# Performance work log

Measured on AMD Instinct MI355X. Metric: run time of the kernel, lower is better.

Reference implementation:

```python
import jax, jax.numpy as jnp
import numpy as np

B, D, U = 64, 256, 256

def setup_inputs() -> dict:
    key = jax.random.key(0)
    ks = jax.random.split(key, 16)
    init_mu = 0.05
    inputs = jax.random.normal(ks[0], (B, D), jnp.float32)
    prev_state = 0.1 * jax.random.normal(ks[1], (B, U), jnp.float32)
    A = jax.random.normal(ks[2], (B, U, U), jnp.float32)
    # symmetric, diagonally boosted covariance-like state
    Sigma_state = 0.01 * (A + jnp.swapaxes(A, 1, 2)) + 0.1 * jnp.eye(U, dtype=jnp.float32)
    def w(k, shape):
        return init_mu * jax.random.normal(k, shape, jnp.float32)
    def s(k):
        return jax.random.uniform(k, (U,), jnp.float32, -4.5, -2.2)
    return {
        'inputs': inputs, 'prev_state': prev_state, 'Sigma_state': Sigma_state,
        'U_z': w(ks[3], (D, U)), 'uz_sigma': s(ks[4]), 'W_z': w(ks[5], (U, U)), 'wz_sigma': s(ks[6]),
        'U_r': w(ks[7], (D, U)), 'ur_sigma': s(ks[8]), 'W_r': w(ks[9], (U, U)), 'wr_sigma': s(ks[10]),
        'U_h': w(ks[11], (D, U)), 'uh_sigma': s(ks[12]), 'W_h': w(ks[13], (U, U)), 'wh_sigma': s(ks[14]),
    }

def _outer(a, b):  # [B,u],[B,u] -> [B,u,u]
    return a[:, :, None] * b[:, None, :]

def _quad(W, S):  # W^T @ S @ W, S is [B,u,u]
    return jnp.matmul(jnp.matmul(W.T, S), W)

def _x_sigma_w(x, sv):  # ||x||^2 * diag(softplus sigma)
    return jnp.sum(x * x, axis=1)[:, None, None] * jnp.diag(sv)

def _tr_sigma_w(S, sv):  # trace(S) * diag(softplus sigma)
    return jnp.trace(S, axis1=1, axis2=2)[:, None, None] * jnp.diag(sv)

def _hadamard_sigma(S1, S2, m1, m2):
    # S1*S2 + diag(m1) S2 diag(m1) + diag(m2) S1 diag(m2) as elementwise/broadcast
    return S1 * S2 + _outer(m1, m1) * S2 + _outer(m2, m2) * S1

def reference(inputs, prev_state, Sigma_state, U_z, uz_sigma, W_z, wz_sigma,
              U_r, ur_sigma, W_r, wr_sigma, U_h, uh_sigma, W_h, wh_sigma):
    sp = jax.nn.softplus
    # --- z gate ---
    az = inputs @ U_z + prev_state @ W_z
    z = jax.nn.sigmoid(az)
    gz = z * (1.0 - z)  # d sigmoid
    Sz = (_quad(W_z, Sigma_state) + _x_sigma_w(prev_state, sp(wz_sigma))
          + _tr_sigma_w(Sigma_state, sp(wz_sigma)) + _x_sigma_w(inputs, sp(uz_sigma)))
    Sigma_out_z = Sz * _outer(gz, gz)
    # --- r gate ---
    ar = inputs @ U_r + prev_state @ W_r
    r = jax.nn.sigmoid(ar)
    gr = r * (1.0 - r)
    Sr = (_quad(W_r, Sigma_state) + _x_sigma_w(prev_state, sp(wr_sigma))
          + _tr_sigma_w(Sigma_state, sp(wr_sigma)) + _x_sigma_w(inputs, sp(ur_sigma)))
    Sigma_out_r = Sr * _outer(gr, gr)
    # --- h candidate ---
    g_in = prev_state * r
    ah = inputs @ U_h + g_in @ W_h
    h = jnp.tanh(ah)
    gh = 1.0 - h * h  # d tanh
    sigma_g = _hadamard_sigma(Sigma_state, Sigma_out_r, prev_state, r)
    Sh = (_quad(W_h, sigma_g) + _x_sigma_w(g_in, sp(wh_sigma))
          + _tr_sigma_w(sigma_g, sp(wh_sigma)) + _x_sigma_w(inputs, sp(uh_sigma)))
    Sigma_out_h = Sh * _outer(gh, gh)
    # --- output combination ---
    mu_out = z * prev_state + (1.0 - z) * h
    sigma_a = _hadamard_sigma(Sigma_out_z, Sigma_state, z, prev_state)
    sigma_b = _hadamard_sigma(Sigma_out_z, Sigma_out_h, 1.0 - z, h)
    Sigma_out = (sigma_a + sigma_b
                 - Sigma_out_z * _outer(prev_state, h)
                 - Sigma_out_z * _outer(h, prev_state))
    Sigma_out = jnp.where(jnp.isnan(Sigma_out) | jnp.isinf(Sigma_out),
                          jnp.zeros_like(Sigma_out), Sigma_out)
    eye = jnp.eye(Sigma_out.shape[-1], dtype=Sigma_out.dtype)
    d = jnp.abs(jnp.diagonal(Sigma_out, axis1=1, axis2=2))
    Sigma_out = Sigma_out * (1.0 - eye) + d[:, :, None] * eye
    return mu_out, Sigma_out
```

## Files before the change

kernel.cpp:

```cpp
#include <hip/hip_runtime.h>
#include <math.h>

#define UDIM 256
#define BATCH 64
#define MATN 65536
#define PITCH 280

typedef __bf16 bf16x8 __attribute__((ext_vector_type(8)));
typedef float  f32x4  __attribute__((ext_vector_type(4)));

__device__ __forceinline__ float softplusf(float x) { return log1pf(expf(x)); }
__device__ __forceinline__ float sigmoidf_(float x) { return 1.f/(1.f+expf(-x)); }

__device__ __forceinline__ bf16x8 frag_load(const __bf16* base, int rt, int kt, int lane) {
  return *(const bf16x8*)(base + (((size_t)(rt*8 + kt))*64 + lane)*8);
}

__device__ __forceinline__ bf16x8 cvt8(const float* p) {
  const float4 f0 = *(const float4*)p;
  const float4 f1 = *(const float4*)(p + 4);
  bf16x8 v;
  v[0]=(__bf16)f0.x; v[1]=(__bf16)f0.y; v[2]=(__bf16)f0.z; v[3]=(__bf16)f0.w;
  v[4]=(__bf16)f1.x; v[5]=(__bf16)f1.y; v[6]=(__bf16)f1.z; v[7]=(__bf16)f1.w;
  return v;
}

__global__ __launch_bounds__(256) void prep_all(
    const float* __restrict__ Uz, const float* __restrict__ Wz,
    const float* __restrict__ Ur, const float* __restrict__ Wr,
    const float* __restrict__ Uh, const float* __restrict__ Wh,
    __bf16* __restrict__ Fw_z, __bf16* __restrict__ Fw_r,
    __bf16* __restrict__ Fu_h, __bf16* __restrict__ Fw_h,
    const float* __restrict__ S, const float* __restrict__ x,
    const float* __restrict__ prev, float* __restrict__ scal,
    __bf16* __restrict__ Sf,
    float* __restrict__ zb, float* __restrict__ rb,
    float* __restrict__ gzb, float* __restrict__ grb,
    float* __restrict__ gin)
{
  const int bid = blockIdx.x;
  const int t = threadIdx.x;
  const int w = t >> 6, l = t & 63, r = l & 15, q = l >> 4;

  __shared__ __align__(16) unsigned char LDSU[16896];

  if (bid < 1024) {
    const int c = bid;
    const int bx = c & 3, by = (c >> 2) & 3, b = c >> 4;
    const size_t sb = (size_t)b * MATN;
#pragma unroll
    for (int ss = 0; ss < 2; ++ss) {
      const int s = t + ss*256;
      const int chunk = s >> 6, lane = s & 63;
      const int rt_l = chunk >> 1, kt_l = chunk & 1;
      const int row = by*64 + rt_l*16 + (lane & 15);
      const int col = bx*64 + kt_l*32 + (lane >> 4)*8;
      const bf16x8 v = cvt8(S + sb + (size_t)row*UDIM + col);
      *(bf16x8*)(Sf + sb + (((size_t)((by*4 + rt_l)*8 + bx*2 + kt_l))*64 + lane)*8) = v;
    }
    return;
  }

  if (bid < 1088) {
    const int u3 = bid - 1024;
    const int mat = u3 >> 4, tl = u3 & 15;
    const int n0 = (tl & 3)*64, k0 = (tl >> 2)*64;
    const float* W; __bf16* F;
    switch (mat) {
      case 0: W = Wz; F = Fw_z; break;  case 1: W = Wr; F = Fw_r; break;
      case 2: W = Uh; F = Fu_h; break;  default: W = Wh; F = Fw_h; break;
    }
    float (*tile)[65] = (float (*)[65])LDSU;
    const int tx = t & 15, ty = t >> 4;
#pragma unroll
    for (int rr = 0; rr < 4; ++rr) {
      const int row = ty*4 + rr;
      const float4 f = *(const float4*)(W + (size_t)(k0 + row)*UDIM + n0 + tx*4);
      tile[row][tx*4+0] = f.x; tile[row][tx*4+1] = f.y;
      tile[row][tx*4+2] = f.z; tile[row][tx*4+3] = f.w;
    }
    __syncthreads();
#pragma unroll
    for (int ss = 0; ss < 2; ++ss) {
      const int s = t + ss*256;
      const int rt_l = s >> 7, kt_l = (s >> 6) & 1, lane = s & 63;
      const int nl = rt_l*16 + (lane & 15), kb = kt_l*32 + (lane >> 4)*8;
      __align__(16) __bf16 tmp[8];
#pragma unroll
      for (int e = 0; e < 8; ++e) tmp[e] = (__bf16)tile[kb + e][nl];
      *(uint4*)(F + (((size_t)((((n0 >> 4) + rt_l)*8) + (k0 >> 5) + kt_l))*64 + lane)*8)
          = *(const uint4*)tmp;
    }
    return;
  }

  if (bid < 1104) {
    const int blk = bid - 1088;
    const int b0 = blk*4 + (t >> 6);
    const float4 xv = *(const float4*)(x + b0*UDIM + l*4);
    float s0 = xv.x*xv.x + xv.y*xv.y + xv.z*xv.z + xv.w*xv.w;
    const float4 pv = *(const float4*)(prev + b0*UDIM + l*4);
    float s1 = pv.x*pv.x + pv.y*pv.y + pv.z*pv.z + pv.w*pv.w;
    float s2 = 0.f;
#pragma unroll
    for (int e = 0; e < 4; ++e)
      s2 += S[(size_t)b0*MATN + (size_t)(l*4 + e)*257];
    for (int off = 32; off; off >>= 1) {
      s0 += __shfl_down(s0, off);
      s1 += __shfl_down(s1, off);
      s2 += __shfl_down(s2, off);
    }
    if (l == 0) { scal[b0] = s0; scal[64 + b0] = s1; scal[128 + b0] = s2; }
    return;
  }

  {
    const int u2 = bid - 1104;
    const int g = u2 >> 4, un = u2 & 15;
    const int jt = un >> 2, ni = un & 3;
    const int n0 = un * 16;
    const float* Um = g ? Ur : Uz;
    const float* Wm = g ? Wr : Wz;
    __bf16 (*Ut)[16][264] = (__bf16 (*)[16][264])LDSU;
    {
      float uv[16], wv[16];
      const float* ur_ = Um + (size_t)t*UDIM + n0;
      const float* wr_ = Wm + (size_t)t*UDIM + n0;
#pragma unroll
      for (int p4 = 0; p4 < 4; ++p4) {
        *(float4*)&uv[p4*4] = *(const float4*)(ur_ + p4*4);
        *(float4*)&wv[p4*4] = *(const float4*)(wr_ + p4*4);
      }
#pragma unroll
      for (int e = 0; e < 16; ++e) {
        Ut[0][e][t] = (__bf16)uv[e];
        Ut[1][e][t] = (__bf16)wv[e];
      }
    }
    __syncthreads();

    const int mrow = w*16 + r;
    f32x4 acc = {};
#pragma unroll
    for (int ks = 0; ks < 16; ++ks) {
      const int k0 = ks*32;
      const float* asrc;
      int src, koff;
      if (k0 < 256) { asrc = x    + (size_t)mrow*UDIM + k0         + q*8; src = 0; koff = k0; }
      else          { asrc = prev + (size_t)mrow*UDIM + (k0 - 256) + q*8; src = 1; koff = k0 - 256; }
      const bf16x8 af = cvt8(asrc);
      const bf16x8 bv = *(const bf16x8*)&Ut[src][r][koff + q*8];
      acc = __builtin_amdgcn_mfma_f32_16x16x32_bf16(af, bv, acc, 0, 0, 0);
    }
    const int n = n0 + r;
    if (g == 0) {
#pragma unroll
      for (int v = 0; v < 4; ++v) {
        const int m = w*16 + q*4 + v;
        const float zv = sigmoidf_(acc[v]);
        zb[m*UDIM + n]  = zv;
        gzb[m*UDIM + n] = zv * (1.f - zv);
      }
    } else {
      float ggp[4];
#pragma unroll
      for (int v = 0; v < 4; ++v) {
        const int m = w*16 + q*4 + v;
        const float rv = sigmoidf_(acc[v]);
        const float pv = prev[m*UDIM + n];
        const float g2 = pv * rv;
        rb[m*UDIM + n]  = rv;
        grb[m*UDIM + n] = rv * (1.f - rv);
        gin[m*UDIM + n] = g2;
        ggp[v] = g2 * g2;
      }
#pragma unroll
      for (int s2 = 1; s2 < 16; s2 <<= 1)
#pragma unroll
        for (int v = 0; v < 4; ++v) ggp[v] += __shfl_xor(ggp[v], s2);
      if (r == 0)
#pragma unroll
        for (int v = 0; v < 4; ++v)
          atomicAdd(&scal[192 + w*16 + q*4 + v], ggp[v]);
    }
  }
}

__global__ __launch_bounds__(256, 4) void quad_zr_gh(
    const float* __restrict__ S, const __bf16* __restrict__ Sf,
    const float* __restrict__ prev,
    const float* __restrict__ rb, const float* __restrict__ gzb,
    const float* __restrict__ grb,
    const float* __restrict__ wz_s, const float* __restrict__ uz_s,
    const float* __restrict__ wr_s, const float* __restrict__ ur_s,
    const __bf16* __restrict__ Fw_z, const __bf16* __restrict__ Fw_r,
    float* __restrict__ scal, __bf16* __restrict__ Szb, __bf16* __restrict__ G,
    const float* __restrict__ x, const float* __restrict__ gin,
    const float* __restrict__ zb,
    const __bf16* __restrict__ Fu_h, const __bf16* __restrict__ Fw_h,
    float* __restrict__ hb, float* __restrict__ ghb, float* __restrict__ mu_out)
{
  const int bid = blockIdx.x;
  const int t = threadIdx.x, w = t >> 6, l = t & 63, r = l & 15, q = l >> 4;

  if (bid < 4) {
    const int jt = bid;
    const int mrow = w*16 + r;
    f32x4 acc[4] = {};
#pragma unroll
    for (int ks = 0; ks < 16; ++ks) {
      const int k0 = ks*32;
      const float* asrc; const __bf16* B; int kk;
      if (k0 < 256) { asrc = x   + (size_t)mrow*UDIM + k0         + q*8; B = Fu_h; kk = k0; }
      else          { asrc = gin + (size_t)mrow*UDIM + (k0 - 256) + q*8; B = Fw_h; kk = k0 - 256; }
      const bf16x8 af = cvt8(asrc);
#pragma unroll
      for (int ni = 0; ni < 4; ++ni) {
        const bf16x8 bv = frag_load(B, jt*4 + ni, kk >> 5, l);
        acc[ni] = __builtin_amdgcn_mfma_f32_16x16x32_bf16(af, bv, acc[ni], 0, 0, 0);
      }
    }
#pragma unroll
    for (int ni = 0; ni < 4; ++ni) {
      const int n = jt*64 + ni*16 + r;
#pragma unroll
      for (int v = 0; v < 4; ++v) {
        const int m = w*16 + q*4 + v;
        const float hv = tanhf(acc[ni][v]);
        const float zv = zb[m*UDIM + n];
        hb[m*UDIM + n]  = hv;
        ghb[m*UDIM + n] = 1.f - hv*hv;
        mu_out[m*UDIM + n] = zv * prev[m*UDIM + n] + (1.f - zv) * hv;
      }
    }
    return;
  }

  const int id = bid - 4;
  const int gater = (id < 1024);
  const int rem = id & 1023;
  const int s = rem >> 6, b = rem & 63;
  const size_t sb = (size_t)b * MATN;
  const __bf16* Sfb = Sf + sb;
  const __bf16* FW = gater ? Fw_r : Fw_z;

  __shared__ __align__(16) __bf16 T[16*PITCH];

  f32x4 a[4] = {};
#pragma unroll
  for (int kt = 0; kt < 8; ++kt) {
    const bf16x8 af = frag_load(FW, s, kt, l);
#pragma unroll
    for (int ct = 0; ct < 4; ++ct) {
      const bf16x8 bv = frag_load(Sfb, w*4 + ct, kt, l);
      a[ct] = __builtin_amdgcn_mfma_f32_16x16x32_bf16(af, bv, a[ct], 0, 0, 0);
    }
  }
#pragma unroll
  for (int ct = 0; ct < 4; ++ct)
#pragma unroll
    for (int v = 0; v < 4; ++v)
      T[(q*4 + v)*PITCH + w*64 + ct*16 + r] = (__bf16)a[ct][v];
  __syncthreads();

  f32x4 qx[4] = {};
#pragma unroll
  for (int kt = 0; kt < 8; ++kt) {
    const bf16x8 at = *(const bf16x8*)&T[r*PITCH + kt*32 + q*8];
#pragma unroll
    for (int ct = 0; ct < 4; ++ct) {
      const bf16x8 bw = frag_load(FW, w*4 + ct, kt, l);
      qx[ct] = __builtin_amdgcn_mfma_f32_16x16x32_bf16(at, bw, qx[ct], 0, 0, 0);
    }
  }

  const float xx = scal[b];
  const float dscal = scal[64 + b] + scal[128 + b];
  const int ib = s*16 + q*4;

  if (!gater) {
    const f32x4 g4 = *(const f32x4*)(gzb + b*UDIM + ib);
    __align__(16) __bf16 o16[16];
#pragma unroll
    for (int ct = 0; ct < 4; ++ct) {
      const int j = (w*4 + ct)*16 + r;
      const float gj = gzb[b*UDIM + j];
#pragma unroll
      for (int v = 0; v < 4; ++v) {
        const int i = ib + v;
        float qv = qx[ct][v];
        if (i == j) qv += dscal*softplusf(wz_s[i]) + xx*softplusf(uz_s[i]);
        o16[ct*4 + v] = (__bf16)(qv * g4[v] * gj);
      }
    }
    __bf16* dst = Szb + ((size_t)(b*16 + s)*256 + t)*16;
    *(uint4*)dst       = *(const uint4*)&o16[0];
    *(uint4*)(dst + 8) = *(const uint4*)&o16[8];
  } else {
    float gvals[16];
    float trg = 0.f;
    {
      const f32x4 g4 = *(const f32x4*)(grb + b*UDIM + ib);
      const f32x4 p4 = *(const f32x4*)(prev + b*UDIM + ib);
      const f32x4 r4 = *(const f32x4*)(rb + b*UDIM + ib);
#pragma unroll
      for (int ct = 0; ct < 4; ++ct) {
        const int j = (w*4 + ct)*16 + r;
        const float gj = grb[b*UDIM + j];
        const float pj = prev[b*UDIM + j];
        const float rj = rb[b*UDIM + j];
#pragma unroll
        for (int v = 0; v < 4; ++v) {
          const int i = ib + v;
          float qv = qx[ct][v];
          if (i == j) qv += dscal*softplusf(wr_s[i]) + xx*softplusf(ur_s[i]);
          const float Sg = qv * g4[v] * gj;
          const float sv = S[sb + (size_t)i*UDIM + j];
          const float go = Sg*(sv + p4[v]*pj) + r4[v]*rj*sv;
          gvals[ct*4 + v] = go;
          if (i == j) trg += go;
        }
      }
    }
    if (trg != 0.f) atomicAdd(&scal[256 + b], trg);

    __syncthreads();
#pragma unroll
    for (int ct = 0; ct < 4; ++ct)
#pragma unroll
      for (int v = 0; v < 4; ++v)
        T[(q*4 + v)*PITCH + w*64 + ct*16 + r] = (__bf16)gvals[ct*4 + v];
    __syncthreads();
#pragma unroll
    for (int ee = 0; ee < 2; ++ee) {
      const int e = t + ee*256;
      const int kt = e >> 6, le = e & 63;
      const uint4 vv = *(const uint4*)&T[(le & 15)*PITCH + kt*32 + (le >> 4)*8];
      *(uint4*)(G + sb + (((size_t)(s*8 + kt))*64 + le)*8) = vv;
    }
  }
}

__global__ __launch_bounds__(256, 4) void quad_h(
    const float* __restrict__ S, const __bf16* __restrict__ Szb,
    const float* __restrict__ prev, const float* __restrict__ zb,
    const float* __restrict__ hb, const float* __restrict__ ghb,
    const float* __restrict__ wh_s, const float* __restrict__ uh_s,
    const __bf16* __restrict__ Fw_h, const __bf16* __restrict__ G,
    const float* __restrict__ scal, float* __restrict__ out_sig)
{
  const int bid = blockIdx.x;
  const int s = bid >> 6, b = bid & 63;
  const size_t sb = (size_t)b * MATN;
  const int t = threadIdx.x, w = t >> 6, l = t & 63, r = l & 15, q = l >> 4;
  const __bf16* Gb = G + sb;

  __shared__ __align__(16) __bf16 Th[16*PITCH];

  f32x4 ah[4] = {};
#pragma unroll
  for (int kt = 0; kt < 8; ++kt) {
    const bf16x8 af = frag_load(Fw_h, s, kt, l);
#pragma unroll
    for (int ct = 0; ct < 4; ++ct) {
      const bf16x8 bv = frag_load(Gb, w*4 + ct, kt, l);
      ah[ct] = __builtin_amdgcn_mfma_f32_16x16x32_bf16(af, bv, ah[ct], 0, 0, 0);
    }
  }
#pragma unroll
  for (int ct = 0; ct < 4; ++ct)
#pragma unroll
    for (int v = 0; v < 4; ++v)
      Th[(q*4 + v)*PITCH + w*64 + ct*16 + r] = (__bf16)ah[ct][v];
  __syncthreads();

  f32x4 qh[4] = {};
#pragma unroll
  for (int kt = 0; kt < 8; ++kt) {
    const bf16x8 at = *(const bf16x8*)&Th[r*PITCH + kt*32 + q*8];
#pragma unroll
    for (int ct = 0; ct < 4; ++ct) {
      const bf16x8 bv = frag_load(Fw_h, w*4 + ct, kt, l);
      qh[ct] = __builtin_amdgcn_mfma_f32_16x16x32_bf16(at, bv, qh[ct], 0, 0, 0);
    }
  }

  const float xx = scal[b];
  const float dscal = scal[192 + b] + scal[256 + b];
  const int ib = s*16 + q*4;

  const __bf16* szp = Szb + ((size_t)(b*16 + s)*256 + t)*16;
  __align__(16) __bf16 sz16[16];
  *(uint4*)&sz16[0] = *(const uint4*)szp;
  *(uint4*)&sz16[8] = *(const uint4*)(szp + 8);

  const f32x4 g4 = *(const f32x4*)(ghb + b*UDIM + ib);
  const f32x4 p4 = *(const f32x4*)(prev + b*UDIM + ib);
  const f32x4 z4 = *(const f32x4*)(zb + b*UDIM + ib);
  const f32x4 h4 = *(const f32x4*)(hb + b*UDIM + ib);

#pragma unroll
  for (int ct = 0; ct < 4; ++ct) {
    const int j = (w*4 + ct)*16 + r;
    const float gj = ghb[b*UDIM + j];
    const float pj = prev[b*UDIM + j];
    const float zj = zb[b*UDIM + j];
    const float hj = hb[b*UDIM + j];
#pragma unroll
    for (int v = 0; v < 4; ++v) {
      const int i = ib + v;
      float qv = qh[ct][v];
      if (i == j) qv += dscal*softplusf(wh_s[i]) + xx*softplusf(uh_s[i]);
      const float Sg = qv * g4[v] * gj;
      const float sv = S[sb + (size_t)i*UDIM + j];
      const float sz = (float)sz16[ct*4 + v];
      float val = sv*(sz + z4[v]*zj)
                + sz*(p4[v] - h4[v])*(pj - hj)
                + Sg*(sz + (1.f - z4[v])*(1.f - zj));
      if (!isfinite(val)) val = 0.f;
      if (i == j) val = fabsf(val);
      out_sig[sb + (size_t)i*UDIM + j] = val;
    }
  }
}

extern "C" void kernel_launch(void* const* d_in, const int* in_sizes, int n_in,
                              void* d_out, int out_size, void* d_ws, size_t ws_size,
                              hipStream_t stream) {
  const float* x    = (const float*)d_in[0];
  const float* prev = (const float*)d_in[1];
  const float* S    = (const float*)d_in[2];
  const float* Uz   = (const float*)d_in[3];
  const float* uz_s = (const float*)d_in[4];
  const float* Wz   = (const float*)d_in[5];
  const float* wz_s = (const float*)d_in[6];
  const float* Ur   = (const float*)d_in[7];
  const float* ur_s = (const float*)d_in[8];
  const float* Wr   = (const float*)d_in[9];
  const float* wr_s = (const float*)d_in[10];
  const float* Uh   = (const float*)d_in[11];
  const float* uh_s = (const float*)d_in[12];
  const float* Wh   = (const float*)d_in[13];
  const float* wh_s = (const float*)d_in[14];

  float* out_mu  = (float*)d_out;
  float* out_sig = out_mu + BATCH*UDIM;

  float* ws   = (float*)d_ws;
  float* zb   = ws;
  float* rb   = zb  + BATCH*UDIM;
  float* gzb  = rb  + BATCH*UDIM;
  float* grb  = gzb + BATCH*UDIM;
  float* gin  = grb + BATCH*UDIM;
  float* hb   = gin + BATCH*UDIM;
  float* ghb  = hb  + BATCH*UDIM;
  float* scal = ghb + BATCH*UDIM;
  __bf16* bws  = (__bf16*)(scal + 512);
  __bf16* Fu_z = bws;
  __bf16* Fw_z = Fu_z + MATN;
  __bf16* Fu_r = Fw_z + MATN;
  __bf16* Fw_r = Fu_r + MATN;
  __bf16* Fu_h = Fw_r + MATN;
  __bf16* Fw_h = Fu_h + MATN;
  const size_t BIG = (size_t)BATCH * MATN;
  __bf16* Szb = Fw_h + MATN;
  __bf16* G   = Szb + BIG;
  __bf16* Sf  = G + BIG;

  (void)hipMemsetAsync(scal, 0, 512*sizeof(float), stream);

  prep_all<<<dim3(1136), 256, 0, stream>>>(Uz, Wz, Ur, Wr, Uh, Wh,
      Fw_z, Fw_r, Fu_h, Fw_h, S, x, prev, scal, Sf,
      zb, rb, gzb, grb, gin);
  quad_zr_gh<<<dim3(2052), 256, 0, stream>>>(S, Sf, prev, rb, gzb, grb,
      wz_s, uz_s, wr_s, ur_s, Fw_z, Fw_r, scal, Szb, G,
      x, gin, zb, Fu_h, Fw_h, hb, ghb, out_mu);
  quad_h<<<dim3(1024), 256, 0, stream>>>(S, Szb, prev, zb, hb, ghb,
      wh_s, uh_s, Fw_h, G, scal, out_sig);
}
```

Measured before the change: 166.0 us.

## Drop bf16 Sigma pre-pack and process two row slabs per block

```diff
diff --git a/kernel.cpp b/kernel.cpp
--- a/kernel.cpp
+++ b/kernel.cpp
@@ -23,6 +23,12 @@
   v[0]=(__bf16)f0.x; v[1]=(__bf16)f0.y; v[2]=(__bf16)f0.z; v[3]=(__bf16)f0.w;
   v[4]=(__bf16)f1.x; v[5]=(__bf16)f1.y; v[6]=(__bf16)f1.z; v[7]=(__bf16)f1.w;
   return v;
+}
+
+__device__ __forceinline__ bf16x8 sfrag(const float* Sb, int rt, int kt, int lane) {
+  const int row = rt*16 + (lane & 15);
+  const int col = kt*32 + (lane >> 4)*8;
+  return cvt8(Sb + (size_t)row*UDIM + col);
 }
 
 __global__ __launch_bounds__(256) void prep_all(
@@ -33,7 +39,6 @@
     __bf16* __restrict__ Fu_h, __bf16* __restrict__ Fw_h,
     const float* __restrict__ S, const float* __restrict__ x,
     const float* __restrict__ prev, float* __restrict__ scal,
-    __bf16* __restrict__ Sf,
     float* __restrict__ zb, float* __restrict__ rb,
     float* __restrict__ gzb, float* __restrict__ grb,
     float* __restrict__ gin)
@@ -44,26 +49,8 @@
 
   __shared__ __align__(16) unsigned char LDSU[16896];
 
-  if (bid < 1024) {
-    const int c = bid;
-    const int bx = c & 3, by = (c >> 2) & 3, b = c >> 4;
-    const size_t sb = (size_t)b * MATN;
-#pragma unroll
-    for (int ss = 0; ss < 2; ++ss) {
-      const int s = t + ss*256;
-      const int chunk = s >> 6, lane = s & 63;
-      const int rt_l = chunk >> 1, kt_l = chunk & 1;
-      const int row = by*64 + rt_l*16 + (lane & 15);
-      const int col = bx*64 + kt_l*32 + (lane >> 4)*8;
-      const bf16x8 v = cvt8(S + sb + (size_t)row*UDIM + col);
-      *(bf16x8*)(Sf + sb + (((size_t)((by*4 + rt_l)*8 + bx*2 + kt_l))*64 + lane)*8) = v;
-    }
-    return;
-  }
-
-  if (bid < 1088) {
-    const int u3 = bid - 1024;
-    const int mat = u3 >> 4, tl = u3 & 15;
+  if (bid < 64) {
+    const int mat = bid >> 4, tl = bid & 15;
     const int n0 = (tl & 3)*64, k0 = (tl >> 2)*64;
     const float* W; __bf16* F;
     switch (mat) {
@@ -94,8 +81,8 @@
     return;
   }
 
-  if (bid < 1104) {
-    const int blk = bid - 1088;
+  if (bid < 80) {
+    const int blk = bid - 64;
     const int b0 = blk*4 + (t >> 6);
     const float4 xv = *(const float4*)(x + b0*UDIM + l*4);
     float s0 = xv.x*xv.x + xv.y*xv.y + xv.z*xv.z + xv.w*xv.w;
@@ -115,9 +102,8 @@
   }
 
   {
-    const int u2 = bid - 1104;
+    const int u2 = bid - 80;
     const int g = u2 >> 4, un = u2 & 15;
-    const int jt = un >> 2, ni = un & 3;
     const int n0 = un * 16;
     const float* Um = g ? Ur : Uz;
     const float* Wm = g ? Wr : Wz;
@@ -187,7 +173,7 @@
 }
 
 __global__ __launch_bounds__(256, 4) void quad_zr_gh(
-    const float* __restrict__ S, const __bf16* __restrict__ Sf,
+    const float* __restrict__ S,
     const float* __restrict__ prev,
     const float* __restrict__ rb, const float* __restrict__ gzb,
     const float* __restrict__ grb,
@@ -237,69 +223,86 @@
   }
 
   const int id = bid - 4;
-  const int gater = (id < 1024);
-  const int rem = id & 1023;
-  const int s = rem >> 6, b = rem & 63;
+  const int gater = (id < 512);
+  const int rem = id & 511;
+  const int sg = rem >> 6, b = rem & 63;
   const size_t sb = (size_t)b * MATN;
-  const __bf16* Sfb = Sf + sb;
+  const float* Sb = S + sb;
   const __bf16* FW = gater ? Fw_r : Fw_z;
 
-  __shared__ __align__(16) __bf16 T[16*PITCH];
-
-  f32x4 a[4] = {};
+  __shared__ __align__(16) __bf16 T[2*16*PITCH];
+
+  f32x4 a[2][4] = {};
 #pragma unroll
   for (int kt = 0; kt < 8; ++kt) {
-    const bf16x8 af = frag_load(FW, s, kt, l);
+    bf16x8 af2[2];
+#pragma unroll
+    for (int sl = 0; sl < 2; ++sl) af2[sl] = frag_load(FW, sg*2 + sl, kt, l);
 #pragma unroll
     for (int ct = 0; ct < 4; ++ct) {
-      const bf16x8 bv = frag_load(Sfb, w*4 + ct, kt, l);
-      a[ct] = __builtin_amdgcn_mfma_f32_16x16x32_bf16(af, bv, a[ct], 0, 0, 0);
-    }
-  }
-#pragma unroll
-  for (int ct = 0; ct < 4; ++ct)
-#pragma unroll
-    for (int v = 0; v < 4; ++v)
-      T[(q*4 + v)*PITCH + w*64 + ct*16 + r] = (__bf16)a[ct][v];
+      const bf16x8 bv = sfrag(Sb, w*4 + ct, kt, l);
+#pragma unroll
+      for (int sl = 0; sl < 2; ++sl)
+        a[sl][ct] = __builtin_amdgcn_mfma_f32_16x16x32_bf16(af2[sl], bv, a[sl][ct], 0, 0, 0);
+    }
+  }
+#pragma unroll
+  for (int sl = 0; sl < 2; ++sl)
+#pragma unroll
+    for (int ct = 0; ct < 4; ++ct)
+#pragma unroll
+      for (int v = 0; v < 4; ++v)
+        T[sl*16*PITCH + (q*4 + v)*PITCH + w*64 + ct*16 + r] = (__bf16)a[sl][ct][v];
   __syncthreads();
 
-  f32x4 qx[4] = {};
+  f32x4 qx[2][4] = {};
 #pragma unroll
   for (int kt = 0; kt < 8; ++kt) {
-    const bf16x8 at = *(const bf16x8*)&T[r*PITCH + kt*32 + q*8];
-#pragma unroll
-    for (int ct = 0; ct < 4; ++ct) {
-      const bf16x8 bw = frag_load(FW, w*4 + ct, kt, l);
-      qx[ct] = __builtin_amdgcn_mfma_f32_16x16x32_bf16(at, bw, qx[ct], 0, 0, 0);
+    bf16x8 bw[4];
+#pragma unroll
+    for (int ct = 0; ct < 4; ++ct) bw[ct] = frag_load(FW, w*4 + ct, kt, l);
+#pragma unroll
+    for (int sl = 0; sl < 2; ++sl) {
+      const bf16x8 at = *(const bf16x8*)&T[sl*16*PITCH + r*PITCH + kt*32 + q*8];
+#pragma unroll
+      for (int ct = 0; ct < 4; ++ct)
+        qx[sl][ct] = __builtin_amdgcn_mfma_f32_16x16x32_bf16(at, bw[ct], qx[sl][ct], 0, 0, 0);
     }
   }
 
   const float xx = scal[b];
   const float dscal = scal[64 + b] + scal[128 + b];
-  const int ib = s*16 + q*4;
 
   if (!gater) {
-    const f32x4 g4 = *(const f32x4*)(gzb + b*UDIM + ib);
-    __align__(16) __bf16 o16[16];
-#pragma unroll
-    for (int ct = 0; ct < 4; ++ct) {
-      const int j = (w*4 + ct)*16 + r;
-      const float gj = gzb[b*UDIM + j];
-#pragma unroll
-      for (int v = 0; v < 4; ++v) {
-        const int i = ib + v;
-        float qv = qx[ct][v];
-        if (i == j) qv += dscal*softplusf(wz_s[i]) + xx*softplusf(uz_s[i]);
-        o16[ct*4 + v] = (__bf16)(qv * g4[v] * gj);
-      }
-    }
-    __bf16* dst = Szb + ((size_t)(b*16 + s)*256 + t)*16;
-    *(uint4*)dst       = *(const uint4*)&o16[0];
-    *(uint4*)(dst + 8) = *(const uint4*)&o16[8];
+#pragma unroll
+    for (int sl = 0; sl < 2; ++sl) {
+      const int s4 = sg*2 + sl;
+      const int ib = s4*16 + q*4;
+      const f32x4 g4 = *(const f32x4*)(gzb + b*UDIM + ib);
+      __align__(16) __bf16 o16[16];
+#pragma unroll
+      for (int ct = 0; ct < 4; ++ct) {
+        const int j = (w*4 + ct)*16 + r;
+        const float gj = gzb[b*UDIM + j];
+#pragma unroll
+        for (int v = 0; v < 4; ++v) {
+          const int i = ib + v;
+          float qv = qx[sl][ct][v];
+          if (i == j) qv += dscal*softplusf(wz_s[i]) + xx*softplusf(uz_s[i]);
+          o16[ct*4 + v] = (__bf16)(qv * g4[v] * gj);
+        }
+      }
+      __bf16* dst = Szb + ((size_t)(b*16 + s4)*256 + t)*16;
+      *(uint4*)dst       = *(const uint4*)&o16[0];
+      *(uint4*)(dst + 8) = *(const uint4*)&o16[8];
+    }
   } else {
-    float gvals[16];
+    __syncthreads();
     float trg = 0.f;
-    {
+#pragma unroll
+    for (int sl = 0; sl < 2; ++sl) {
+      const int s4 = sg*2 + sl;
+      const int ib = s4*16 + q*4;
       const f32x4 g4 = *(const f32x4*)(grb + b*UDIM + ib);
       const f32x4 p4 = *(const f32x4*)(prev + b*UDIM + ib);
       const f32x4 r4 = *(const f32x4*)(rb + b*UDIM + ib);
@@ -312,32 +315,27 @@
 #pragma unroll
         for (int v = 0; v < 4; ++v) {
           const int i = ib + v;
-          float qv = qx[ct][v];
+          float qv = qx[sl][ct][v];
           if (i == j) qv += dscal*softplusf(wr_s[i]) + xx*softplusf(ur_s[i]);
           const float Sg = qv * g4[v] * gj;
-          const float sv = S[sb + (size_t)i*UDIM + j];
+          const float sv = Sb[(size_t)i*UDIM + j];
           const float go = Sg*(sv + p4[v]*pj) + r4[v]*rj*sv;
-          gvals[ct*4 + v] = go;
+          T[sl*16*PITCH + (q*4 + v)*PITCH + w*64 + ct*16 + r] = (__bf16)go;
           if (i == j) trg += go;
         }
       }
     }
     if (trg != 0.f) atomicAdd(&scal[256 + b], trg);
-
     __syncthreads();
 #pragma unroll
-    for (int ct = 0; ct < 4; ++ct)
-#pragma unroll
-      for (int v = 0; v < 4; ++v)
-        T[(q*4 + v)*PITCH + w*64 + ct*16 + r] = (__bf16)gvals[ct*4 + v];
-    __syncthreads();
-#pragma unroll
-    for (int ee = 0; ee < 2; ++ee) {
-      const int e = t + ee*256;
-      const int kt = e >> 6, le = e & 63;
-      const uint4 vv = *(const uint4*)&T[(le & 15)*PITCH + kt*32 + (le >> 4)*8];
-      *(uint4*)(G + sb + (((size_t)(s*8 + kt))*64 + le)*8) = vv;
-    }
+    for (int sl = 0; sl < 2; ++sl)
+#pragma unroll
+      for (int ee = 0; ee < 2; ++ee) {
+        const int e = t + ee*256;
+        const int kt = e >> 6, le = e & 63;
+        const uint4 vv = *(const uint4*)&T[sl*16*PITCH + (le & 15)*PITCH + kt*32 + (le >> 4)*8];
+        *(uint4*)(G + sb + (((size_t)((sg*2 + sl)*8 + kt))*64 + le)*8) = vv;
+      }
   }
 }
 
@@ -350,76 +348,91 @@
     const float* __restrict__ scal, float* __restrict__ out_sig)
 {
   const int bid = blockIdx.x;
-  const int s = bid >> 6, b = bid & 63;
+  const int sg = bid >> 6, b = bid & 63;
   const size_t sb = (size_t)b * MATN;
   const int t = threadIdx.x, w = t >> 6, l = t & 63, r = l & 15, q = l >> 4;
   const __bf16* Gb = G + sb;
 
-  __shared__ __align__(16) __bf16 Th[16*PITCH];
-
-  f32x4 ah[4] = {};
+  __shared__ __align__(16) __bf16 Th[2*16*PITCH];
+
+  f32x4 ah[2][4] = {};
 #pragma unroll
   for (int kt = 0; kt < 8; ++kt) {
-    const bf16x8 af = frag_load(Fw_h, s, kt, l);
+    bf16x8 af2[2];
+#pragma unroll
+    for (int sl = 0; sl < 2; ++sl) af2[sl] = frag_load(Fw_h, sg*2 + sl, kt, l);
 #pragma unroll
     for (int ct = 0; ct < 4; ++ct) {
       const bf16x8 bv = frag_load(Gb, w*4 + ct, kt, l);
-      ah[ct] = __builtin_amdgcn_mfma_f32_16x16x32_bf16(af, bv, ah[ct], 0, 0, 0);
-    }
-  }
-#pragma unroll
-  for (int ct = 0; ct < 4; ++ct)
-#pragma unroll
-    for (int v = 0; v < 4; ++v)
-      Th[(q*4 + v)*PITCH + w*64 + ct*16 + r] = (__bf16)ah[ct][v];
+#pragma unroll
+      for (int sl = 0; sl < 2; ++sl)
+        ah[sl][ct] = __builtin_amdgcn_mfma_f32_16x16x32_bf16(af2[sl], bv, ah[sl][ct], 0, 0, 0);
+    }
+  }
+#pragma unroll
+  for (int sl = 0; sl < 2; ++sl)
+#pragma unroll
+    for (int ct = 0; ct < 4; ++ct)
+#pragma unroll
+      for (int v = 0; v < 4; ++v)
+        Th[sl*16*PITCH + (q*4 + v)*PITCH + w*64 + ct*16 + r] = (__bf16)ah[sl][ct][v];
   __syncthreads();
 
-  f32x4 qh[4] = {};
+  f32x4 qh[2][4] = {};
 #pragma unroll
   for (int kt = 0; kt < 8; ++kt) {
-    const bf16x8 at = *(const bf16x8*)&Th[r*PITCH + kt*32 + q*8];
-#pragma unroll
-    for (int ct = 0; ct < 4; ++ct) {
-      const bf16x8 bv = frag_load(Fw_h, w*4 + ct, kt, l);
-      qh[ct] = __builtin_amdgcn_mfma_f32_16x16x32_bf16(at, bv, qh[ct], 0, 0, 0);
+    bf16x8 bw2[4];
+#pragma unroll
+    for (int ct = 0; ct < 4; ++ct) bw2[ct] = frag_load(Fw_h, w*4 + ct, kt, l);
+#pragma unroll
+    for (int sl = 0; sl < 2; ++sl) {
+      const bf16x8 at = *(const bf16x8*)&Th[sl*16*PITCH + r*PITCH + kt*32 + q*8];
+#pragma unroll
+      for (int ct = 0; ct < 4; ++ct)
+        qh[sl][ct] = __builtin_amdgcn_mfma_f32_16x16x32_bf16(at, bw2[ct], qh[sl][ct], 0, 0, 0);
     }
   }
 
   const float xx = scal[b];
   const float dscal = scal[192 + b] + scal[256 + b];
-  const int ib = s*16 + q*4;
-
-  const __bf16* szp = Szb + ((size_t)(b*16 + s)*256 + t)*16;
-  __align__(16) __bf16 sz16[16];
-  *(uint4*)&sz16[0] = *(const uint4*)szp;
-  *(uint4*)&sz16[8] = *(const uint4*)(szp + 8);
-
-  const f32x4 g4 = *(const f32x4*)(ghb + b*UDIM + ib);
-  const f32x4 p4 = *(const f32x4*)(prev + b*UDIM + ib);
-  const f32x4 z4 = *(const f32x4*)(zb + b*UDIM + ib);
-  const f32x4 h4 = *(const f32x4*)(hb + b*UDIM + ib);
-
-#pragma unroll
-  for (int ct = 0; ct < 4; ++ct) {
-    const int j = (w*4 + ct)*16 + r;
-    const float gj = ghb[b*UDIM + j];
-    const float pj = prev[b*UDIM + j];
-    const float zj = zb[b*UDIM + j];
-    const float hj = hb[b*UDIM + j];
-#pragma unroll
-    for (int v = 0; v < 4; ++v) {
-      const int i = ib + v;
-      float qv = qh[ct][v];
-      if (i == j) qv += dscal*softplusf(wh_s[i]) + xx*softplusf(uh_s[i]);
-      const float Sg = qv * g4[v] * gj;
-      const float sv = S[sb + (size_t)i*UDIM + j];
-      const float sz = (float)sz16[ct*4 + v];
-      float val = sv*(sz + z4[v]*zj)
-                + sz*(p4[v] - h4[v])*(pj - hj)
-                + Sg*(sz + (1.f - z4[v])*(1.f - zj));
-      if (!isfinite(val)) val = 0.f;
-      if (i == j) val = fabsf(val);
-      out_sig[sb + (size_t)i*UDIM + j] = val;
+
+#pragma unroll
+  for (int sl = 0; sl < 2; ++sl) {
+    const int s4 = sg*2 + sl;
+    const int ib = s4*16 + q*4;
+
+    const __bf16* szp = Szb + ((size_t)(b*16 + s4)*256 + t)*16;
+    __align__(16) __bf16 sz16[16];
+    *(uint4*)&sz16[0] = *(const uint4*)szp;
+    *(uint4*)&sz16[8] = *(const uint4*)(szp + 8);
+
+    const f32x4 g4 = *(const f32x4*)(ghb + b*UDIM + ib);
+    const f32x4 p4 = *(const f32x4*)(prev + b*UDIM + ib);
+    const f32x4 z4 = *(const f32x4*)(zb + b*UDIM + ib);
+    const f32x4 h4 = *(const f32x4*)(hb + b*UDIM + ib);
+
+#pragma unroll
+    for (int ct = 0; ct < 4; ++ct) {
+      const int j = (w*4 + ct)*16 + r;
+      const float gj = ghb[b*UDIM + j];
+      const float pj = prev[b*UDIM + j];
+      const float zj = zb[b*UDIM + j];
+      const float hj = hb[b*UDIM + j];
+#pragma unroll
+      for (int v = 0; v < 4; ++v) {
+        const int i = ib + v;
+        float qv = qh[sl][ct][v];
+        if (i == j) qv += dscal*softplusf(wh_s[i]) + xx*softplusf(uh_s[i]);
+        const float Sg = qv * g4[v] * gj;
+        const float sv = S[sb + (size_t)i*UDIM + j];
+        const float sz = (float)sz16[ct*4 + v];
+        float val = sv*(sz + z4[v]*zj)
+                  + sz*(p4[v] - h4[v])*(pj - hj)
+                  + Sg*(sz + (1.f - z4[v])*(1.f - zj));
+        if (!isfinite(val)) val = 0.f;
+        if (i == j) val = fabsf(val);
+        out_sig[sb + (size_t)i*UDIM + j] = val;
+      }
     }
   }
 }
@@ -456,25 +469,22 @@
   float* ghb  = hb  + BATCH*UDIM;
   float* scal = ghb + BATCH*UDIM;
   __bf16* bws  = (__bf16*)(scal + 512);
-  __bf16* Fu_z = bws;
-  __bf16* Fw_z = Fu_z + MATN;
-  __bf16* Fu_r = Fw_z + MATN;
-  __bf16* Fw_r = Fu_r + MATN;
+  __bf16* Fw_z = bws;
+  __bf16* Fw_r = Fw_z + MATN;
   __bf16* Fu_h = Fw_r + MATN;
   __bf16* Fw_h = Fu_h + MATN;
   const size_t BIG = (size_t)BATCH * MATN;
   __bf16* Szb = Fw_h + MATN;
   __bf16* G   = Szb + BIG;
-  __bf16* Sf  = G + BIG;
 
   (void)hipMemsetAsync(scal, 0, 512*sizeof(float), stream);
 
-  prep_all<<<dim3(1136), 256, 0, stream>>>(Uz, Wz, Ur, Wr, Uh, Wh,
-      Fw_z, Fw_r, Fu_h, Fw_h, S, x, prev, scal, Sf,
+  prep_all<<<dim3(112), 256, 0, stream>>>(Uz, Wz, Ur, Wr, Uh, Wh,
+      Fw_z, Fw_r, Fu_h, Fw_h, S, x, prev, scal,
       zb, rb, gzb, grb, gin);
-  quad_zr_gh<<<dim3(2052), 256, 0, stream>>>(S, Sf, prev, rb, gzb, grb,
+  quad_zr_gh<<<dim3(1028), 256, 0, stream>>>(S, prev, rb, gzb, grb,
       wz_s, uz_s, wr_s, ur_s, Fw_z, Fw_r, scal, Szb, G,
       x, gin, zb, Fu_h, Fw_h, hb, ghb, out_mu);
-  quad_h<<<dim3(1024), 256, 0, stream>>>(S, Szb, prev, zb, hb, ghb,
+  quad_h<<<dim3(512), 256, 0, stream>>>(S, Szb, prev, zb, hb, ghb,
       wh_s, uh_s, Fw_h, G, scal, out_sig);
 }
```

Result: slower. 178.9 us (+7.7%).

## Compute z and r gate quadratic forms in one block sharing Sigma fragments

Applied to the files above, without the earlier changes.

```diff
diff --git a/kernel.cpp b/kernel.cpp
--- a/kernel.cpp
+++ b/kernel.cpp
@@ -117,7 +117,6 @@
   {
     const int u2 = bid - 1104;
     const int g = u2 >> 4, un = u2 & 15;
-    const int jt = un >> 2, ni = un & 3;
     const int n0 = un * 16;
     const float* Um = g ? Ur : Uz;
     const float* Wm = g ? Wr : Wz;
@@ -237,40 +236,46 @@
   }
 
   const int id = bid - 4;
-  const int gater = (id < 1024);
-  const int rem = id & 1023;
-  const int s = rem >> 6, b = rem & 63;
+  const int s = id >> 6, b = id & 63;
   const size_t sb = (size_t)b * MATN;
   const __bf16* Sfb = Sf + sb;
-  const __bf16* FW = gater ? Fw_r : Fw_z;
-
-  __shared__ __align__(16) __bf16 T[16*PITCH];
-
-  f32x4 a[4] = {};
+
+  __shared__ __align__(16) __bf16 T[2*16*PITCH];
+  __bf16* Tz = T;
+  __bf16* Tr = T + 16*PITCH;
+
+  f32x4 az[4] = {}, ar[4] = {};
 #pragma unroll
   for (int kt = 0; kt < 8; ++kt) {
-    const bf16x8 af = frag_load(FW, s, kt, l);
+    const bf16x8 wzf = frag_load(Fw_z, s, kt, l);
+    const bf16x8 wrf = frag_load(Fw_r, s, kt, l);
 #pragma unroll
     for (int ct = 0; ct < 4; ++ct) {
       const bf16x8 bv = frag_load(Sfb, w*4 + ct, kt, l);
-      a[ct] = __builtin_amdgcn_mfma_f32_16x16x32_bf16(af, bv, a[ct], 0, 0, 0);
+      az[ct] = __builtin_amdgcn_mfma_f32_16x16x32_bf16(wzf, bv, az[ct], 0, 0, 0);
+      ar[ct] = __builtin_amdgcn_mfma_f32_16x16x32_bf16(wrf, bv, ar[ct], 0, 0, 0);
     }
   }
 #pragma unroll
   for (int ct = 0; ct < 4; ++ct)
 #pragma unroll
-    for (int v = 0; v < 4; ++v)
-      T[(q*4 + v)*PITCH + w*64 + ct*16 + r] = (__bf16)a[ct][v];
+    for (int v = 0; v < 4; ++v) {
+      Tz[(q*4 + v)*PITCH + w*64 + ct*16 + r] = (__bf16)az[ct][v];
+      Tr[(q*4 + v)*PITCH + w*64 + ct*16 + r] = (__bf16)ar[ct][v];
+    }
   __syncthreads();
 
-  f32x4 qx[4] = {};
+  f32x4 qz[4] = {}, qr[4] = {};
 #pragma unroll
   for (int kt = 0; kt < 8; ++kt) {
-    const bf16x8 at = *(const bf16x8*)&T[r*PITCH + kt*32 + q*8];
+    const bf16x8 atz = *(const bf16x8*)&Tz[r*PITCH + kt*32 + q*8];
+    const bf16x8 atr = *(const bf16x8*)&Tr[r*PITCH + kt*32 + q*8];
 #pragma unroll
     for (int ct = 0; ct < 4; ++ct) {
-      const bf16x8 bw = frag_load(FW, w*4 + ct, kt, l);
-      qx[ct] = __builtin_amdgcn_mfma_f32_16x16x32_bf16(at, bw, qx[ct], 0, 0, 0);
+      const bf16x8 bwz = frag_load(Fw_z, w*4 + ct, kt, l);
+      const bf16x8 bwr = frag_load(Fw_r, w*4 + ct, kt, l);
+      qz[ct] = __builtin_amdgcn_mfma_f32_16x16x32_bf16(atz, bwz, qz[ct], 0, 0, 0);
+      qr[ct] = __builtin_amdgcn_mfma_f32_16x16x32_bf16(atr, bwr, qr[ct], 0, 0, 0);
     }
   }
 
@@ -278,7 +283,7 @@
   const float dscal = scal[64 + b] + scal[128 + b];
   const int ib = s*16 + q*4;
 
-  if (!gater) {
+  {
     const f32x4 g4 = *(const f32x4*)(gzb + b*UDIM + ib);
     __align__(16) __bf16 o16[16];
 #pragma unroll
@@ -288,7 +293,7 @@
 #pragma unroll
       for (int v = 0; v < 4; ++v) {
         const int i = ib + v;
-        float qv = qx[ct][v];
+        float qv = qz[ct][v];
         if (i == j) qv += dscal*softplusf(wz_s[i]) + xx*softplusf(uz_s[i]);
         o16[ct*4 + v] = (__bf16)(qv * g4[v] * gj);
       }
@@ -296,7 +301,9 @@
     __bf16* dst = Szb + ((size_t)(b*16 + s)*256 + t)*16;
     *(uint4*)dst       = *(const uint4*)&o16[0];
     *(uint4*)(dst + 8) = *(const uint4*)&o16[8];
-  } else {
+  }
+
+  {
     float gvals[16];
     float trg = 0.f;
     {
@@ -312,7 +319,7 @@
 #pragma unroll
         for (int v = 0; v < 4; ++v) {
           const int i = ib + v;
-          float qv = qx[ct][v];
+          float qv = qr[ct][v];
           if (i == j) qv += dscal*softplusf(wr_s[i]) + xx*softplusf(ur_s[i]);
           const float Sg = qv * g4[v] * gj;
           const float sv = S[sb + (size_t)i*UDIM + j];
@@ -329,13 +336,13 @@
     for (int ct = 0; ct < 4; ++ct)
 #pragma unroll
       for (int v = 0; v < 4; ++v)
-        T[(q*4 + v)*PITCH + w*64 + ct*16 + r] = (__bf16)gvals[ct*4 + v];
+        Tr[(q*4 + v)*PITCH + w*64 + ct*16 + r] = (__bf16)gvals[ct*4 + v];
     __syncthreads();
 #pragma unroll
     for (int ee = 0; ee < 2; ++ee) {
       const int e = t + ee*256;
       const int kt = e >> 6, le = e & 63;
-      const uint4 vv = *(const uint4*)&T[(le & 15)*PITCH + kt*32 + (le >> 4)*8];
+      const uint4 vv = *(const uint4*)&Tr[(le & 15)*PITCH + kt*32 + (le >> 4)*8];
       *(uint4*)(G + sb + (((size_t)(s*8 + kt))*64 + le)*8) = vv;
     }
   }
@@ -456,10 +463,8 @@
   float* ghb  = hb  + BATCH*UDIM;
   float* scal = ghb + BATCH*UDIM;
   __bf16* bws  = (__bf16*)(scal + 512);
-  __bf16* Fu_z = bws;
-  __bf16* Fw_z = Fu_z + MATN;
-  __bf16* Fu_r = Fw_z + MATN;
-  __bf16* Fw_r = Fu_r + MATN;
+  __bf16* Fw_z = bws;
+  __bf16* Fw_r = Fw_z + MATN;
   __bf16* Fu_h = Fw_r + MATN;
   __bf16* Fw_h = Fu_h + MATN;
   const size_t BIG = (size_t)BATCH * MATN;
@@ -472,7 +477,7 @@
   prep_all<<<dim3(1136), 256, 0, stream>>>(Uz, Wz, Ur, Wr, Uh, Wh,
       Fw_z, Fw_r, Fu_h, Fw_h, S, x, prev, scal, Sf,
       zb, rb, gzb, grb, gin);
-  quad_zr_gh<<<dim3(2052), 256, 0, stream>>>(S, Sf, prev, rb, gzb, grb,
+  quad_zr_gh<<<dim3(1028), 256, 0, stream>>>(S, Sf, prev, rb, gzb, grb,
       wz_s, uz_s, wr_s, ur_s, Fw_z, Fw_r, scal, Szb, G,
       x, gin, zb, Fu_h, Fw_h, hb, ghb, out_mu);
   quad_h<<<dim3(1024), 256, 0, stream>>>(S, Szb, prev, zb, hb, ghb,
```

Result: no change. 167.3 us (+0.7%).
